# Optimization experiments

Hardware: AMD Instinct MI355X
Metric: run time of the kernel (lower is better)

The kernel has to match this reference:

```python
import jax, jax.numpy as jnp
import numpy as np


def setup_inputs() -> dict:
    key = jax.random.key(0)
    k1, k2 = jax.random.split(key)
    imgs = jax.random.normal(k1, (8, 32, 256, 256), dtype=jnp.float32)
    kernel = jax.random.normal(k2, (32, 1, 5, 5), dtype=jnp.float32)
    return {
        "imgs": imgs,
        "kernel": kernel,
        "stride": 1,
        "padding": 2,
        "dilation": 1,
        "groups": 32,
    }


def reference(imgs, kernel, stride, padding, dilation, groups):
    """Tropical (max-plus) select-semifield convolution (correlation layout).

    out[b, oc, oy, ox] = max over (g, ky, kx) of
        imgs[b, ic, oy*stride - pad + ky*dil, ox*stride - pad + kx*dil]
        + kernel[oc_in_group, g, ky, kx]
    with ic = (oc // per_group_out) * krn_cs + g. Out-of-bounds taps are
    skipped (neutral element -inf), matching the CUDA kernel's bounds check.
    """
    B, C, H, W = imgs.shape
    OC, KC, KY, KX = kernel.shape  # KC = krn_cs = C // groups
    per_group_out = OC // groups
    out_h = (H + 2 * padding - dilation * (KY - 1) - 1) // stride + 1
    out_w = (W + 2 * padding - dilation * (KX - 1) - 1) // stride + 1

    neutral = -jnp.inf  # semifield neutral for max-plus
    padded = jnp.pad(
        imgs,
        ((0, 0), (0, 0), (padding, padding), (padding, padding)),
        constant_values=neutral,
    )

    oc = jnp.arange(OC)
    acc = jnp.full((B, OC, out_h, out_w), neutral, dtype=imgs.dtype)
    for g in range(KC):  # fixed small loop over kernel taps (krn_cs * KY * KX)
        ic = (oc // per_group_out) * KC + g
        img_g = padded[:, ic]  # [B, OC, H+2p, W+2p] aligned to output channels
        for ky in range(KY):
            ys = slice(ky * dilation, ky * dilation + stride * (out_h - 1) + 1, stride)
            for kx in range(KX):
                xs = slice(kx * dilation, kx * dilation + stride * (out_w - 1) + 1, stride)
                k = kernel[:, g, ky, kx][None, :, None, None]  # [1, OC, 1, 1]
                acc = jnp.maximum(acc, img_g[:, :, ys, xs] + k)
    return acc
```

## Files before the change

### kernel.cpp

```cpp
#include <hip/hip_runtime.h>
#include <math.h>

#define BB 8
#define CC 32
#define HH 256
#define WW 256

__global__ __launch_bounds__(256, 4) void selconv_kernel(
    const float* __restrict__ imgs,
    const float* __restrict__ kern,
    float* __restrict__ out)
{
    const int t    = threadIdx.x;
    const int lane = t & 63;
    const int wave = __builtin_amdgcn_readfirstlane((int)blockIdx.x * 4 + (t >> 6));
    const int p    = wave >> 5;
    const int rt   = wave & 31;
    const int c    = p & (CC - 1);
    const int y0   = rt * 8;
    const int x    = lane * 4;

    float w[25];
    const float* kw = kern + c * 25;
#pragma unroll
    for (int i = 0; i < 25; ++i) w[i] = kw[i];

    const float NEG = -INFINITY;
    const float* plane = imgs + (size_t)p * (HH * WW);

    const bool okL = (lane != 0);
    const bool okR = (lane != 63);
    const int  xl  = okL ? x - 2 : 0;
    const int  xr  = okR ? x + 4 : WW - 4;

    float acc[8][4];
#pragma unroll
    for (int r = 0; r < 8; ++r)
#pragma unroll
        for (int j = 0; j < 4; ++j) acc[r][j] = NEG;

    auto dorow = [&](int iyo) {
        const float* rp = plane + (y0 + iyo) * WW;
        const float2 L = *reinterpret_cast<const float2*>(rp + xl);
        const float4 M = *reinterpret_cast<const float4*>(rp + x);
        const float2 R = *reinterpret_cast<const float2*>(rp + xr);
        float v[8];
        v[0] = okL ? L.x : NEG;  v[1] = okL ? L.y : NEG;
        v[2] = M.x;  v[3] = M.y;  v[4] = M.z;  v[5] = M.w;
        v[6] = okR ? R.x : NEG;  v[7] = okR ? R.y : NEG;
#pragma unroll
        for (int ky = 0; ky < 5; ++ky) {
            const int r = iyo + 2 - ky;
            if (r < 0 || r > 7) continue;
#pragma unroll
            for (int j = 0; j < 4; ++j) {
                const float s0 = v[j + 0] + w[ky * 5 + 0];
                const float s1 = v[j + 1] + w[ky * 5 + 1];
                const float s2 = v[j + 2] + w[ky * 5 + 2];
                const float s3 = v[j + 3] + w[ky * 5 + 3];
                const float s4 = v[j + 4] + w[ky * 5 + 4];
                acc[r][j] = fmaxf(fmaxf(fmaxf(s0, s1), s2),
                                  fmaxf(fmaxf(s3, s4), acc[r][j]));
            }
        }
    };

    if (rt != 0 && rt != 31) {
#pragma unroll
        for (int iyo = -2; iyo <= 9; ++iyo) dorow(iyo);
    } else {
#pragma unroll
        for (int iyo = -2; iyo <= 9; ++iyo) {
            const int iy = y0 + iyo;
            if (iy < 0 || iy >= HH) continue;
            dorow(iyo);
        }
    }

    float* op = out + (size_t)p * (HH * WW) + y0 * WW + x;
#pragma unroll
    for (int r = 0; r < 8; ++r) {
        *reinterpret_cast<float4*>(op + r * WW) =
            make_float4(acc[r][0], acc[r][1], acc[r][2], acc[r][3]);
    }
}

extern "C" void kernel_launch(void* const* d_in, const int* in_sizes, int n_in,
                              void* d_out, int out_size, void* d_ws, size_t ws_size,
                              hipStream_t stream)
{
    const float* imgs = (const float*)d_in[0];
    const float* kern = (const float*)d_in[1];
    float* out = (float*)d_out;

    const int blocks = (BB * CC * (HH / 8) * (WW / 4)) / 256;
    selconv_kernel<<<blocks, 256, 0, stream>>>(imgs, kern, out);
}
```

Measured before the change: 30.83 us.

## Stage 16-row input tiles in LDS via direct global-to-LDS loads

Each 256-thread block now covers a 16-row strip of one plane. It loads the 20 halo-padded rows into LDS with global_load_lds and fills rows outside the plane with -inf. Each wave then computes 4 output rows from 8 LDS rows, instead of each wave reading 12 rows from global memory for 8 outputs. This cuts redundant global halo reads and register pressure, so the launch bound rises to 8 blocks. In exchange it adds LDS traffic, a block barrier, and 20KB of LDS per block, which may limit occupancy.

```diff
diff --git a/kernel.cpp b/kernel.cpp
--- a/kernel.cpp
+++ b/kernel.cpp
@@ -5,81 +5,106 @@
 #define CC 32
 #define HH 256
 #define WW 256
+#define TR 16
+#define LR (TR + 4)
 
-__global__ __launch_bounds__(256, 4) void selconv_kernel(
+typedef unsigned int u32;
+
+__global__ __launch_bounds__(256, 8) void selconv_kernel(
     const float* __restrict__ imgs,
     const float* __restrict__ kern,
     float* __restrict__ out)
 {
+    __shared__ float lds[LR * WW];
+
     const int t    = threadIdx.x;
     const int lane = t & 63;
-    const int wave = __builtin_amdgcn_readfirstlane((int)blockIdx.x * 4 + (t >> 6));
-    const int p    = wave >> 5;
-    const int rt   = wave & 31;
+    const int wv   = t >> 6;
+    const int p    = blockIdx.x >> 4;
+    const int rt   = blockIdx.x & 15;
     const int c    = p & (CC - 1);
-    const int y0   = rt * 8;
+    const int y0   = rt * TR;
     const int x    = lane * 4;
+
+    const float NEG = -INFINITY;
+    const float* plane = imgs + (size_t)p * (HH * WW);
+
+    if (rt != 0 && rt != 15) {
+#pragma unroll
+        for (int i = 0; i < 5; ++i) {
+            const int L  = wv * 5 + i;
+            const int iy = y0 - 2 + L;
+            __builtin_amdgcn_global_load_lds(
+                (const __attribute__((address_space(1))) u32*)(plane + iy * WW + lane * 4),
+                (__attribute__((address_space(3))) u32*)(&lds[L * WW]),
+                16, 0, 0);
+        }
+    } else {
+#pragma unroll
+        for (int i = 0; i < 5; ++i) {
+            const int L  = wv * 5 + i;
+            const int iy = y0 - 2 + L;
+            if (iy >= 0 && iy < HH) {
+                __builtin_amdgcn_global_load_lds(
+                    (const __attribute__((address_space(1))) u32*)(plane + iy * WW + lane * 4),
+                    (__attribute__((address_space(3))) u32*)(&lds[L * WW]),
+                    16, 0, 0);
+            } else {
+                *reinterpret_cast<float4*>(&lds[L * WW + lane * 4]) =
+                    make_float4(NEG, NEG, NEG, NEG);
+            }
+        }
+    }
 
     float w[25];
     const float* kw = kern + c * 25;
 #pragma unroll
     for (int i = 0; i < 25; ++i) w[i] = kw[i];
 
-    const float NEG = -INFINITY;
-    const float* plane = imgs + (size_t)p * (HH * WW);
+    __syncthreads();
 
+    const int or0 = wv * 4;
     const bool okL = (lane != 0);
     const bool okR = (lane != 63);
-    const int  xl  = okL ? x - 2 : 0;
-    const int  xr  = okR ? x + 4 : WW - 4;
+    const int  xl  = okL ? x - 4 : 0;
+    const int  xr  = okR ? x + 4 : 0;
 
-    float acc[8][4];
+    float acc[4][4];
 #pragma unroll
-    for (int r = 0; r < 8; ++r)
+    for (int r = 0; r < 4; ++r)
 #pragma unroll
         for (int j = 0; j < 4; ++j) acc[r][j] = NEG;
 
-    auto dorow = [&](int iyo) {
-        const float* rp = plane + (y0 + iyo) * WW;
-        const float2 L = *reinterpret_cast<const float2*>(rp + xl);
-        const float4 M = *reinterpret_cast<const float4*>(rp + x);
-        const float2 R = *reinterpret_cast<const float2*>(rp + xr);
-        float v[8];
-        v[0] = okL ? L.x : NEG;  v[1] = okL ? L.y : NEG;
-        v[2] = M.x;  v[3] = M.y;  v[4] = M.z;  v[5] = M.w;
-        v[6] = okR ? R.x : NEG;  v[7] = okR ? R.y : NEG;
+#pragma unroll
+    for (int dl = 0; dl < 8; ++dl) {
+        const float* lrow = &lds[(or0 + dl) * WW];
+        const float4 A = *reinterpret_cast<const float4*>(lrow + xl);
+        const float4 M = *reinterpret_cast<const float4*>(lrow + x);
+        const float4 R = *reinterpret_cast<const float4*>(lrow + xr);
+        float v[10];
+        v[2] = okL ? A.z : NEG;  v[3] = okL ? A.w : NEG;
+        v[4] = M.x;  v[5] = M.y;  v[6] = M.z;  v[7] = M.w;
+        v[8] = okR ? R.x : NEG;  v[9] = okR ? R.y : NEG;
 #pragma unroll
         for (int ky = 0; ky < 5; ++ky) {
-            const int r = iyo + 2 - ky;
-            if (r < 0 || r > 7) continue;
+            const int r = dl - ky;
+            if (r < 0 || r > 3) continue;
 #pragma unroll
             for (int j = 0; j < 4; ++j) {
-                const float s0 = v[j + 0] + w[ky * 5 + 0];
-                const float s1 = v[j + 1] + w[ky * 5 + 1];
-                const float s2 = v[j + 2] + w[ky * 5 + 2];
-                const float s3 = v[j + 3] + w[ky * 5 + 3];
-                const float s4 = v[j + 4] + w[ky * 5 + 4];
+                const float s0 = v[j + 2] + w[ky * 5 + 0];
+                const float s1 = v[j + 3] + w[ky * 5 + 1];
+                const float s2 = v[j + 4] + w[ky * 5 + 2];
+                const float s3 = v[j + 5] + w[ky * 5 + 3];
+                const float s4 = v[j + 6] + w[ky * 5 + 4];
                 acc[r][j] = fmaxf(fmaxf(fmaxf(s0, s1), s2),
                                   fmaxf(fmaxf(s3, s4), acc[r][j]));
             }
         }
-    };
-
-    if (rt != 0 && rt != 31) {
-#pragma unroll
-        for (int iyo = -2; iyo <= 9; ++iyo) dorow(iyo);
-    } else {
-#pragma unroll
-        for (int iyo = -2; iyo <= 9; ++iyo) {
-            const int iy = y0 + iyo;
-            if (iy < 0 || iy >= HH) continue;
-            dorow(iyo);
-        }
     }
 
-    float* op = out + (size_t)p * (HH * WW) + y0 * WW + x;
+    float* op = out + (size_t)p * (HH * WW) + (y0 + or0) * WW + x;
 #pragma unroll
-    for (int r = 0; r < 8; ++r) {
+    for (int r = 0; r < 4; ++r) {
         *reinterpret_cast<float4*>(op + r * WW) =
             make_float4(acc[r][0], acc[r][1], acc[r][2], acc[r][3]);
     }
@@ -93,6 +118,6 @@
     const float* kern = (const float*)d_in[1];
     float* out = (float*)d_out;
 
-    const int blocks = (BB * CC * (HH / 8) * (WW / 4)) / 256;
+    const int blocks = BB * CC * (HH / TR);
     selconv_kernel<<<blocks, 256, 0, stream>>>(imgs, kern, out);
 }
```

Measured after the change: 30.35 us. Within noise of the previous version (-1.6%).
